# Optimization experiments

Hardware: AMD Instinct MI355X
Metric: run time of the kernel (lower is better)

## Reference

```python
import jax, jax.numpy as jnp
import numpy as np

B, NIN, NOUT, E = 4, 50000, 50000, 819200
CIN, COUT, H = 16, 16, 100


def _lin(key, fan_in, fan_out):
    k1, k2 = jax.random.split(key)
    s = 1.0 / np.sqrt(fan_in)
    w = jax.random.uniform(k1, (fan_in, fan_out), jnp.float32, -s, s)
    b = jax.random.uniform(k2, (fan_out,), jnp.float32, -s, s)
    return w, b


def setup_inputs() -> dict:
    key = jax.random.key(0)
    ks = jax.random.split(key, 12)
    inp = {}
    inp["x"] = jax.random.normal(ks[0], (B, NIN * CIN), jnp.float32)
    inp["inp_positions"] = jax.random.uniform(ks[1], (NIN, 3), jnp.float32)
    inp["out_positions"] = jax.random.uniform(ks[2], (NOUT, 3), jnp.float32)
    inp["edge_src"] = jax.random.randint(ks[3], (E,), 0, NIN)
    inp["edge_dst"] = jax.random.randint(ks[4], (E,), 0, NOUT)
    # edge-MLP: Linear(6,100) -> ReLU -> Linear(100,100) -> ReLU -> Linear(100,100) -> ReLU -> Linear(100, CIN*COUT)
    inp["w1"], inp["b1"] = _lin(ks[5], 6, H)
    inp["w2"], inp["b2"] = _lin(ks[6], H, H)
    inp["w3"], inp["b3"] = _lin(ks[7], H, H)
    inp["w4"], inp["b4"] = _lin(ks[8], H, CIN * COUT)
    inp["root"], _ = _lin(ks[9], CIN, COUT)  # NNConv root weight
    inp["bias"] = jax.random.uniform(ks[10], (COUT,), jnp.float32, -0.05, 0.05)
    return inp


def reference(x, inp_positions, out_positions, w1, b1, w2, b2, w3, b3, w4, b4, root, bias, edge_src, edge_dst):
    # x: (B, NIN*CIN) -> node features of input nodes; output nodes get zero features
    xb = x.reshape(B, NIN, CIN)
    # edge attributes: cat(out_pos[dst], in_pos[src]) -> (E, 6)
    e_attr = jnp.concatenate([out_positions[edge_dst], inp_positions[edge_src]], axis=1)
    # per-edge MLP producing edge-conditioned weight matrix (E, CIN, COUT)
    h = jax.nn.relu(e_attr @ w1 + b1)
    h = jax.nn.relu(h @ w2 + b2)
    h = jax.nn.relu(h @ w3 + b3)
    W = (h @ w4 + b4).reshape(E, CIN, COUT)
    # gather source features, apply edge-specific matmul -> messages (E, B, COUT)
    x_src = xb[:, edge_src]  # (B, E, CIN)
    msg = jnp.einsum('bei,eio->ebo', x_src, W)
    # mean-aggregate into destination (output) nodes
    agg = jax.ops.segment_sum(msg.reshape(E, B * COUT), edge_dst, num_segments=NOUT)
    deg = jax.ops.segment_sum(jnp.ones((E,), jnp.float32), edge_dst, num_segments=NOUT)
    agg = (agg / jnp.clip(deg, 1.0)[:, None]).reshape(NOUT, B, COUT)
    # root-weight term: destination node features are zeros -> contributes zero; bias remains
    out = jnp.transpose(agg, (1, 0, 2)) + bias  # (B, NOUT, COUT)
    return out
```

## Files before the change

### kernel.cpp

```cpp
#include <hip/hip_runtime.h>
#include <hip/hip_bf16.h>
#include <cstdint>

constexpr int B_    = 4;
constexpr int NIN_  = 50000;
constexpr int NOUT_ = 50000;
constexpr int E_    = 819200;
constexpr int CI    = 16;
constexpr int CO    = 16;
constexpr int Hh    = 100;

constexpr int NBLK   = 256;
constexpr int BITER  = E_ / 512;
constexpr size_t LDS_BYTES = 163840;

typedef __attribute__((ext_vector_type(8))) short bf16x8;
typedef __attribute__((ext_vector_type(4))) float f32x4;

union frag { bf16x8 v; unsigned u[4]; };

__device__ inline unsigned pk2(float a, float b) {
    unsigned r;
    asm("v_cvt_pk_bf16_f32 %0, %1, %2" : "=v"(r) : "v"(a), "v"(b));
    return r;
}

__device__ inline int chunkXor(int r) { return ((r & 7) << 3) ^ ((r & 8) << 1); }
__device__ inline int swz(int r, int k) { return r * 128 + (k ^ chunkXor(r)); }


__global__ __launch_bounds__(256)
void prep_kernel(const float* __restrict__ w1, const float* __restrict__ w2,
                 const float* __restrict__ w3, const float* __restrict__ w4,
                 const float* __restrict__ b1, const float* __restrict__ b2,
                 const float* __restrict__ b3, const float* __restrict__ b4,
                 unsigned short* __restrict__ wcat, unsigned short* __restrict__ W1T,
                 float* __restrict__ b1p, float* __restrict__ b2p,
                 float* __restrict__ b3p, float* __restrict__ b4p)
{
    const int i = blockIdx.x * 256 + threadIdx.x;
    auto bf = [](float f) {
        __hip_bfloat16 h = __float2bfloat16(f);
        return *reinterpret_cast<unsigned short*>(&h);
    };
    auto inv = [](int kpos) {
        return ((kpos >> 2) & 1) * 64 + ((kpos >> 5) & 3) * 16 +
               ((kpos >> 3) & 3) * 4 + (kpos & 3);
    };
    if (i < 32768) {
        int j = i & 16383; int r = j >> 7, kz = j & 127;
        int kpos = kz ^ chunkXor(r);
        int u = inv(kpos);
        const float* w = (i < 16384) ? w2 : w3;
        wcat[i] = (r < Hh && u < Hh) ? bf(w[u * Hh + r]) : (unsigned short)0;
    } else if (i < 65536) {
        int j = i - 32768; int r = j >> 7, kz = j & 127;
        int kpos = kz ^ chunkXor(r);
        int u = inv(kpos);
        wcat[i] = (u < Hh) ? bf(w4[u * 256 + r]) : (unsigned short)0;
    } else if (i < 69632) {
        int j = i - 65536; int wi = j >> 5, k = j & 31;
        W1T[j] = (k < 6 && wi < Hh) ? bf(w1[k * Hh + wi]) : (unsigned short)0;
    } else if (i < 69760) { int j = i - 69632; b1p[j] = (j < Hh) ? b1[j] : 0.f; }
    else if (i < 69888) { int j = i - 69760; b2p[j] = (j < Hh) ? b2[j] : 0.f; }
    else if (i < 70016) { int j = i - 69888; b3p[j] = (j < Hh) ? b3[j] : 0.f; }
    else if (i < 70272) { int j = i - 70016; b4p[j] = b4[j]; }
}

__global__ __launch_bounds__(256)
void packx_kernel(const float* __restrict__ x, uint4* __restrict__ xbf4)
{
    const int s = blockIdx.x * 256 + threadIdx.x;
    if (s >= NIN_) return;
    float4 r[4][4];
    #pragma unroll
    for (int b = 0; b < 4; ++b) {
        const float* xp = x + ((size_t)b * NIN_ + s) * CI;
        #pragma unroll
        for (int q = 0; q < 4; ++q)
            r[b][q] = *reinterpret_cast<const float4*>(xp + q * 4);
    }
    #pragma unroll
    for (int p = 0; p < 8; ++p) {
        const int q = p >> 1;
        const int h = (p & 1) * 2;
        uint4 v;
        v.x = pk2(((const float*)&r[0][q])[h],     ((const float*)&r[1][q])[h]);
        v.y = pk2(((const float*)&r[2][q])[h],     ((const float*)&r[3][q])[h]);
        v.z = pk2(((const float*)&r[0][q])[h + 1], ((const float*)&r[1][q])[h + 1]);
        v.w = pk2(((const float*)&r[2][q])[h + 1], ((const float*)&r[3][q])[h + 1]);
        xbf4[(size_t)s * 8 + p] = v;
    }
}

__device__ inline void hidden_layer4(const unsigned short* __restrict__ Wl,
                                     const float* __restrict__ bp,
                                     const frag (&in)[4][4], frag (&out)[4][4],
                                     int cl, int kg)
{
    #pragma unroll
    for (int nt = 0; nt < 8; ++nt) {
        bf16x8 wf[4];
        #pragma unroll
        for (int ks = 0; ks < 4; ++ks)
            wf[ks] = *reinterpret_cast<const bf16x8*>(
                Wl + swz(nt * 16 + cl, ks * 32 + kg * 8));
        f32x4 bias = *reinterpret_cast<const f32x4*>(bp + nt * 16 + kg * 4);
        #pragma unroll
        for (int et = 0; et < 4; ++et) {
            f32x4 acc = bias;
            #pragma unroll
            for (int ks = 0; ks < 4; ++ks)
                acc = __builtin_amdgcn_mfma_f32_16x16x32_bf16(wf[ks], in[et][ks].v, acc, 0, 0, 0);
            out[et][nt & 3].u[((nt >> 2) << 1) + 0] = pk2(fmaxf(acc[0], 0.f), fmaxf(acc[1], 0.f));
            out[et][nt & 3].u[((nt >> 2) << 1) + 1] = pk2(fmaxf(acc[2], 0.f), fmaxf(acc[3], 0.f));
        }
    }
}

__global__ __launch_bounds__(512)
__attribute__((amdgpu_waves_per_eu(2, 2)))
void edge_kernel(const uint4* __restrict__ xbf4, const float* __restrict__ ipos,
                 const float* __restrict__ opos, const int* __restrict__ esrc,
                 const int* __restrict__ edst,
                 const unsigned short* __restrict__ wcat,
                 const unsigned short* __restrict__ W1T,
                 const float* __restrict__ b1p, const float* __restrict__ b2p,
                 const float* __restrict__ b3p, const float* __restrict__ b4p,
                 float* __restrict__ agg, float* __restrict__ deg)
{
    extern __shared__ char lds[];
    unsigned short* Wlds = (unsigned short*)lds;

    const int tid  = threadIdx.x;
    const int wv   = __builtin_amdgcn_readfirstlane(tid >> 6);
    const int lane = tid & 63;
    const int cl   = lane & 15;
    const int kg   = lane >> 4;

    int srcv, dstv; unsigned au0, au1, au2;
    {
        const int eA = (blockIdx.x * 8 + wv) * 64 + lane;
        srcv = esrc[eA]; dstv = edst[eA];
        atomicAdd(&deg[dstv], 1.0f);
        float o0 = opos[dstv * 3 + 0], o1 = opos[dstv * 3 + 1], o2 = opos[dstv * 3 + 2];
        float i0 = ipos[srcv * 3 + 0], i1 = ipos[srcv * 3 + 1], i2 = ipos[srcv * 3 + 2];
        au0 = pk2(o0, o1); au1 = pk2(o2, i0); au2 = pk2(i1, i2);
    }

    {
        const float4* s4 = (const float4*)wcat;
        float4* d4 = (float4*)lds;
        for (int i = tid; i < 8192; i += 512) d4[i] = s4[i];
    }
    __syncthreads();

    uint2* xs = (uint2*)(lds + 131072 + wv * 4096);

    for (int bt = blockIdx.x; bt < BITER; bt += NBLK) {
        uint4 xq[8];
        {
            const uint4* xp = xbf4 + (size_t)srcv * 8;
            #pragma unroll
            for (int p = 0; p < 8; ++p) xq[p] = xp[p];
        }
        bf16x8 a1w[8];
        #pragma unroll
        for (int nt = 0; nt < 8; ++nt)
            a1w[nt] = *reinterpret_cast<const bf16x8*>(
                W1T + (nt * 16 + cl) * 32 + kg * 8);

        frag b1f[4];
        #pragma unroll
        for (int et = 0; et < 4; ++et) {
            const int sl = et * 16 + cl;
            unsigned s0 = __shfl(au0, sl), s1 = __shfl(au1, sl), s2 = __shfl(au2, sl);
            frag f;
            f.u[0] = (kg == 0) ? s0 : 0u;
            f.u[1] = (kg == 0) ? s1 : 0u;
            f.u[2] = (kg == 0) ? s2 : 0u;
            f.u[3] = 0u;
            b1f[et] = f;
        }

        frag B2[4][4];
        #pragma unroll
        for (int nt = 0; nt < 8; ++nt) {
            f32x4 bias = *reinterpret_cast<const f32x4*>(b1p + nt * 16 + kg * 4);
            #pragma unroll
            for (int et = 0; et < 4; ++et) {
                f32x4 acc = bias;
                acc = __builtin_amdgcn_mfma_f32_16x16x32_bf16(a1w[nt], b1f[et].v, acc, 0, 0, 0);
                B2[et][nt & 3].u[((nt >> 2) << 1) + 0] = pk2(fmaxf(acc[0], 0.f), fmaxf(acc[1], 0.f));
                B2[et][nt & 3].u[((nt >> 2) << 1) + 1] = pk2(fmaxf(acc[2], 0.f), fmaxf(acc[3], 0.f));
            }
        }

        int nsrc = srcv, ndst = dstv;
        unsigned na0 = au0, na1 = au1, na2 = au2;
        {
            const int nbt = bt + NBLK;
            if (nbt < BITER) {
                const int neA = (nbt * 8 + wv) * 64 + lane;
                nsrc = esrc[neA]; ndst = edst[neA];
                atomicAdd(&deg[ndst], 1.0f);
                float o0 = opos[ndst * 3 + 0], o1 = opos[ndst * 3 + 1], o2 = opos[ndst * 3 + 2];
                float i0 = ipos[nsrc * 3 + 0], i1 = ipos[nsrc * 3 + 1], i2 = ipos[nsrc * 3 + 2];
                na0 = pk2(o0, o1); na1 = pk2(o2, i0); na2 = pk2(i1, i2);
            }
        }

        frag B3[4][4];
        hidden_layer4(Wlds, b2p, B2, B3, cl, kg);
        frag B4[4][4];
        hidden_layer4(Wlds + 16384, b3p, B3, B4, cl, kg);

        float macc[4][16];
        #pragma unroll
        for (int et = 0; et < 4; ++et)
            #pragma unroll
            for (int q = 0; q < 16; ++q) macc[et][q] = 0.f;

        const unsigned short* W4l = Wlds + 32768;

        #pragma unroll
        for (int p = 0; p < 4; ++p) {
            xs[(2 * p + 0) * 64 + lane] = make_uint2(xq[p].x, xq[p].y);
            xs[(2 * p + 1) * 64 + lane] = make_uint2(xq[p].z, xq[p].w);
        }
        #pragma unroll
        for (int nt = 0; nt < 8; ++nt) {
            bf16x8 wf[4];
            #pragma unroll
            for (int ks = 0; ks < 4; ++ks)
                wf[ks] = *reinterpret_cast<const bf16x8*>(
                    W4l + swz(nt * 16 + cl, ks * 32 + kg * 8));
            const float bv = b4p[nt * 16 + cl];
            #pragma unroll
            for (int et = 0; et < 4; ++et) {
                const uint4 xa = *reinterpret_cast<const uint4*>(
                    &xs[nt * 64 + et * 16 + kg * 4]);
                const uint4 xb = *reinterpret_cast<const uint4*>(
                    &xs[nt * 64 + et * 16 + kg * 4 + 2]);
                f32x4 acc = {bv, bv, bv, bv};
                #pragma unroll
                for (int ks = 0; ks < 4; ++ks)
                    acc = __builtin_amdgcn_mfma_f32_16x16x32_bf16(B4[et][ks].v, wf[ks], acc, 0, 0, 0);
                const unsigned w01b[4] = {xa.x, xa.z, xb.x, xb.z};
                const unsigned w23b[4] = {xa.y, xa.w, xb.y, xb.w};
                #pragma unroll
                for (int j = 0; j < 4; ++j) {
                    const float x0 = __uint_as_float(w01b[j] << 16);
                    const float x1 = __uint_as_float(w01b[j] & 0xffff0000u);
                    const float x2 = __uint_as_float(w23b[j] << 16);
                    const float x3 = __uint_as_float(w23b[j] & 0xffff0000u);
                    macc[et][0 * 4 + j] = fmaf(x0, acc[j], macc[et][0 * 4 + j]);
                    macc[et][1 * 4 + j] = fmaf(x1, acc[j], macc[et][1 * 4 + j]);
                    macc[et][2 * 4 + j] = fmaf(x2, acc[j], macc[et][2 * 4 + j]);
                    macc[et][3 * 4 + j] = fmaf(x3, acc[j], macc[et][3 * 4 + j]);
                }
            }
        }

        #pragma unroll
        for (int p = 0; p < 4; ++p) {
            xs[(2 * p + 0) * 64 + lane] = make_uint2(xq[4 + p].x, xq[4 + p].y);
            xs[(2 * p + 1) * 64 + lane] = make_uint2(xq[4 + p].z, xq[4 + p].w);
        }
        #pragma unroll
        for (int nt8 = 0; nt8 < 8; ++nt8) {
            const int nt = 8 + nt8;
            bf16x8 wf[4];
            #pragma unroll
            for (int ks = 0; ks < 4; ++ks)
                wf[ks] = *reinterpret_cast<const bf16x8*>(
                    W4l + swz(nt * 16 + cl, ks * 32 + kg * 8));
            const float bv = b4p[nt * 16 + cl];
            #pragma unroll
            for (int et = 0; et < 4; ++et) {
                const uint4 xa = *reinterpret_cast<const uint4*>(
                    &xs[nt8 * 64 + et * 16 + kg * 4]);
                const uint4 xb = *reinterpret_cast<const uint4*>(
                    &xs[nt8 * 64 + et * 16 + kg * 4 + 2]);
                f32x4 acc = {bv, bv, bv, bv};
                #pragma unroll
                for (int ks = 0; ks < 4; ++ks)
                    acc = __builtin_amdgcn_mfma_f32_16x16x32_bf16(B4[et][ks].v, wf[ks], acc, 0, 0, 0);
                const unsigned w01b[4] = {xa.x, xa.z, xb.x, xb.z};
                const unsigned w23b[4] = {xa.y, xa.w, xb.y, xb.w};
                #pragma unroll
                for (int j = 0; j < 4; ++j) {
                    const float x0 = __uint_as_float(w01b[j] << 16);
                    const float x1 = __uint_as_float(w01b[j] & 0xffff0000u);
                    const float x2 = __uint_as_float(w23b[j] << 16);
                    const float x3 = __uint_as_float(w23b[j] & 0xffff0000u);
                    macc[et][0 * 4 + j] = fmaf(x0, acc[j], macc[et][0 * 4 + j]);
                    macc[et][1 * 4 + j] = fmaf(x1, acc[j], macc[et][1 * 4 + j]);
                    macc[et][2 * 4 + j] = fmaf(x2, acc[j], macc[et][2 * 4 + j]);
                    macc[et][3 * 4 + j] = fmaf(x3, acc[j], macc[et][3 * 4 + j]);
                }
            }
        }

        #pragma unroll
        for (int et = 0; et < 4; ++et)
            #pragma unroll
            for (int j = 0; j < 4; ++j) {
                const int d = __shfl(dstv, et * 16 + kg * 4 + j);
                #pragma unroll
                for (int b = 0; b < 4; ++b)
                    atomicAdd(agg + (size_t)b * (NOUT_ * CO) + (size_t)d * CO + cl,
                              macc[et][b * 4 + j]);
            }

        srcv = nsrc; dstv = ndst; au0 = na0; au1 = na1; au2 = na2;
    }
}

__global__ __launch_bounds__(256)
void finalize_kernel(const float* __restrict__ agg, const float* __restrict__ deg,
                     const float* __restrict__ bias, float* __restrict__ out)
{
    const int idx4 = blockIdx.x * 256 + threadIdx.x;
    const int n = (idx4 >> 2) % NOUT_;
    const float4 a = reinterpret_cast<const float4*>(agg)[idx4];
    const float dinv = 1.0f / fmaxf(deg[n], 1.0f);
    const float4 bv = reinterpret_cast<const float4*>(bias)[idx4 & 3];
    float4 o;
    o.x = a.x * dinv + bv.x;
    o.y = a.y * dinv + bv.y;
    o.z = a.z * dinv + bv.z;
    o.w = a.w * dinv + bv.w;
    reinterpret_cast<float4*>(out)[idx4] = o;
}

extern "C" void kernel_launch(void* const* d_in, const int* in_sizes, int n_in,
                              void* d_out, int out_size, void* d_ws, size_t ws_size,
                              hipStream_t stream)
{
    const float* x    = (const float*)d_in[0];
    const float* ipos = (const float*)d_in[1];
    const float* opos = (const float*)d_in[2];
    const int*   esrc = (const int*)d_in[3];
    const int*   edst = (const int*)d_in[4];
    const float* w1   = (const float*)d_in[5];
    const float* b1   = (const float*)d_in[6];
    const float* w2   = (const float*)d_in[7];
    const float* b2   = (const float*)d_in[8];
    const float* w3   = (const float*)d_in[9];
    const float* b3   = (const float*)d_in[10];
    const float* w4   = (const float*)d_in[11];
    const float* b4   = (const float*)d_in[12];
    const float* bias = (const float*)d_in[14];

    char* ob = (char*)d_out;
    unsigned short* wcat = (unsigned short*)ob;
    unsigned short* W1T  = (unsigned short*)(ob + 131072);
    float* b1p = (float*)(ob + 139264);
    float* b2p = (float*)(ob + 139776);
    float* b3p = (float*)(ob + 140288);
    float* b4p = (float*)(ob + 140800);
    uint4* xbf4 = (uint4*)(ob + 147456);

    float* agg = (float*)d_ws;
    float* deg = agg + (size_t)B_ * NOUT_ * CO;

    hipMemsetAsync(d_ws, 0,
                   ((size_t)B_ * NOUT_ * CO + NOUT_) * sizeof(float), stream);

    prep_kernel<<<275, 256, 0, stream>>>(w1, w2, w3, w4, b1, b2, b3, b4,
                                         wcat, W1T, b1p, b2p, b3p, b4p);
    packx_kernel<<<(NIN_ + 255) / 256, 256, 0, stream>>>(x, xbf4);

    hipFuncSetAttribute(reinterpret_cast<const void*>(edge_kernel),
                        hipFuncAttributeMaxDynamicSharedMemorySize,
                        (int)LDS_BYTES);
    edge_kernel<<<NBLK, 512, LDS_BYTES, stream>>>(
        xbf4, ipos, opos, esrc, edst, wcat, W1T, b1p, b2p, b3p, b4p, agg, deg);

    finalize_kernel<<<B_ * NOUT_ * CO / 4 / 256, 256, 0, stream>>>(
        agg, deg, bias, (float*)d_out);
}
```

Before: 363.0 us.

## Stream W4 from global memory to halve LDS and double occupancy

Only the W2/W3 weights are now staged in LDS, and the last-layer weight W4 is read straight from global memory (through the cache), which cuts the LDS footprint in half. That allows twice as many blocks (NBLK 512) and waves_per_eu 4. The per-wave x staging buffer shrinks to a 4-row ring that is refilled chunk by chunk. The trade-off is a lower register budget per wave, with possible spills, plus W4 fragment loads that now come from global/L1 instead of LDS.

```diff
diff --git a/kernel.cpp b/kernel.cpp
--- a/kernel.cpp
+++ b/kernel.cpp
@@ -10,9 +10,9 @@
 constexpr int CO    = 16;
 constexpr int Hh    = 100;
 
-constexpr int NBLK   = 256;
+constexpr int NBLK   = 512;
 constexpr int BITER  = E_ / 512;
-constexpr size_t LDS_BYTES = 163840;
+constexpr size_t LDS_BYTES = 81920;
 
 typedef __attribute__((ext_vector_type(8))) short bf16x8;
 typedef __attribute__((ext_vector_type(4))) float f32x4;
@@ -119,7 +119,7 @@
 }
 
 __global__ __launch_bounds__(512)
-__attribute__((amdgpu_waves_per_eu(2, 2)))
+__attribute__((amdgpu_waves_per_eu(4, 4)))
 void edge_kernel(const uint4* __restrict__ xbf4, const float* __restrict__ ipos,
                  const float* __restrict__ opos, const int* __restrict__ esrc,
                  const int* __restrict__ edst,
@@ -151,11 +151,12 @@
     {
         const float4* s4 = (const float4*)wcat;
         float4* d4 = (float4*)lds;
-        for (int i = tid; i < 8192; i += 512) d4[i] = s4[i];
+        for (int i = tid; i < 4096; i += 512) d4[i] = s4[i];
     }
     __syncthreads();
 
-    uint2* xs = (uint2*)(lds + 131072 + wv * 4096);
+    uint2* xs = (uint2*)(lds + 65536 + wv * 2048);
+    const unsigned short* W4g = wcat + 32768;
 
     for (int bt = blockIdx.x; bt < BITER; bt += NBLK) {
         uint4 xq[8];
@@ -221,83 +222,49 @@
             #pragma unroll
             for (int q = 0; q < 16; ++q) macc[et][q] = 0.f;
 
-        const unsigned short* W4l = Wlds + 32768;
-
-        #pragma unroll
-        for (int p = 0; p < 4; ++p) {
-            xs[(2 * p + 0) * 64 + lane] = make_uint2(xq[p].x, xq[p].y);
-            xs[(2 * p + 1) * 64 + lane] = make_uint2(xq[p].z, xq[p].w);
-        }
-        #pragma unroll
-        for (int nt = 0; nt < 8; ++nt) {
-            bf16x8 wf[4];
-            #pragma unroll
-            for (int ks = 0; ks < 4; ++ks)
-                wf[ks] = *reinterpret_cast<const bf16x8*>(
-                    W4l + swz(nt * 16 + cl, ks * 32 + kg * 8));
-            const float bv = b4p[nt * 16 + cl];
-            #pragma unroll
-            for (int et = 0; et < 4; ++et) {
-                const uint4 xa = *reinterpret_cast<const uint4*>(
-                    &xs[nt * 64 + et * 16 + kg * 4]);
-                const uint4 xb = *reinterpret_cast<const uint4*>(
-                    &xs[nt * 64 + et * 16 + kg * 4 + 2]);
-                f32x4 acc = {bv, bv, bv, bv};
+        xs[0 * 64 + lane] = make_uint2(xq[0].x, xq[0].y);
+        xs[1 * 64 + lane] = make_uint2(xq[0].z, xq[0].w);
+
+        #pragma unroll
+        for (int c = 0; c < 8; ++c) {
+            if (c < 7) {
+                const int r0 = 2 * ((c + 1) & 1);
+                xs[(r0 + 0) * 64 + lane] = make_uint2(xq[c + 1].x, xq[c + 1].y);
+                xs[(r0 + 1) * 64 + lane] = make_uint2(xq[c + 1].z, xq[c + 1].w);
+            }
+            #pragma unroll
+            for (int j2 = 0; j2 < 2; ++j2) {
+                const int nt = 2 * c + j2;
+                bf16x8 wf[4];
                 #pragma unroll
                 for (int ks = 0; ks < 4; ++ks)
-                    acc = __builtin_amdgcn_mfma_f32_16x16x32_bf16(B4[et][ks].v, wf[ks], acc, 0, 0, 0);
-                const unsigned w01b[4] = {xa.x, xa.z, xb.x, xb.z};
-                const unsigned w23b[4] = {xa.y, xa.w, xb.y, xb.w};
+                    wf[ks] = *reinterpret_cast<const bf16x8*>(
+                        W4g + swz(nt * 16 + cl, ks * 32 + kg * 8));
+                const float bv = b4p[nt * 16 + cl];
+                const int xrow = (nt & 3) * 64;
                 #pragma unroll
-                for (int j = 0; j < 4; ++j) {
-                    const float x0 = __uint_as_float(w01b[j] << 16);
-                    const float x1 = __uint_as_float(w01b[j] & 0xffff0000u);
-                    const float x2 = __uint_as_float(w23b[j] << 16);
-                    const float x3 = __uint_as_float(w23b[j] & 0xffff0000u);
-                    macc[et][0 * 4 + j] = fmaf(x0, acc[j], macc[et][0 * 4 + j]);
-                    macc[et][1 * 4 + j] = fmaf(x1, acc[j], macc[et][1 * 4 + j]);
-                    macc[et][2 * 4 + j] = fmaf(x2, acc[j], macc[et][2 * 4 + j]);
-                    macc[et][3 * 4 + j] = fmaf(x3, acc[j], macc[et][3 * 4 + j]);
-                }
-            }
-        }
-
-        #pragma unroll
-        for (int p = 0; p < 4; ++p) {
-            xs[(2 * p + 0) * 64 + lane] = make_uint2(xq[4 + p].x, xq[4 + p].y);
-            xs[(2 * p + 1) * 64 + lane] = make_uint2(xq[4 + p].z, xq[4 + p].w);
-        }
-        #pragma unroll
-        for (int nt8 = 0; nt8 < 8; ++nt8) {
-            const int nt = 8 + nt8;
-            bf16x8 wf[4];
-            #pragma unroll
-            for (int ks = 0; ks < 4; ++ks)
-                wf[ks] = *reinterpret_cast<const bf16x8*>(
-                    W4l + swz(nt * 16 + cl, ks * 32 + kg * 8));
-            const float bv = b4p[nt * 16 + cl];
-            #pragma unroll
-            for (int et = 0; et < 4; ++et) {
-                const uint4 xa = *reinterpret_cast<const uint4*>(
-                    &xs[nt8 * 64 + et * 16 + kg * 4]);
-                const uint4 xb = *reinterpret_cast<const uint4*>(
-                    &xs[nt8 * 64 + et * 16 + kg * 4 + 2]);
-                f32x4 acc = {bv, bv, bv, bv};
-                #pragma unroll
-                for (int ks = 0; ks < 4; ++ks)
-                    acc = __builtin_amdgcn_mfma_f32_16x16x32_bf16(B4[et][ks].v, wf[ks], acc, 0, 0, 0);
-                const unsigned w01b[4] = {xa.x, xa.z, xb.x, xb.z};
-                const unsigned w23b[4] = {xa.y, xa.w, xb.y, xb.w};
-                #pragma unroll
-                for (int j = 0; j < 4; ++j) {
-                    const float x0 = __uint_as_float(w01b[j] << 16);
-                    const float x1 = __uint_as_float(w01b[j] & 0xffff0000u);
-                    const float x2 = __uint_as_float(w23b[j] << 16);
-                    const float x3 = __uint_as_float(w23b[j] & 0xffff0000u);
-                    macc[et][0 * 4 + j] = fmaf(x0, acc[j], macc[et][0 * 4 + j]);
-                    macc[et][1 * 4 + j] = fmaf(x1, acc[j], macc[et][1 * 4 + j]);
-                    macc[et][2 * 4 + j] = fmaf(x2, acc[j], macc[et][2 * 4 + j]);
-                    macc[et][3 * 4 + j] = fmaf(x3, acc[j], macc[et][3 * 4 + j]);
+                for (int et = 0; et < 4; ++et) {
+                    const uint4 xa = *reinterpret_cast<const uint4*>(
+                        &xs[xrow + et * 16 + kg * 4]);
+                    const uint4 xb = *reinterpret_cast<const uint4*>(
+                        &xs[xrow + et * 16 + kg * 4 + 2]);
+                    f32x4 acc = {bv, bv, bv, bv};
+                    #pragma unroll
+                    for (int ks = 0; ks < 4; ++ks)
+                        acc = __builtin_amdgcn_mfma_f32_16x16x32_bf16(B4[et][ks].v, wf[ks], acc, 0, 0, 0);
+                    const unsigned w01b[4] = {xa.x, xa.z, xb.x, xb.z};
+                    const unsigned w23b[4] = {xa.y, xa.w, xb.y, xb.w};
+                    #pragma unroll
+                    for (int j = 0; j < 4; ++j) {
+                        const float x0 = __uint_as_float(w01b[j] << 16);
+                        const float x1 = __uint_as_float(w01b[j] & 0xffff0000u);
+                        const float x2 = __uint_as_float(w23b[j] << 16);
+                        const float x3 = __uint_as_float(w23b[j] & 0xffff0000u);
+                        macc[et][0 * 4 + j] = fmaf(x0, acc[j], macc[et][0 * 4 + j]);
+                        macc[et][1 * 4 + j] = fmaf(x1, acc[j], macc[et][1 * 4 + j]);
+                        macc[et][2 * 4 + j] = fmaf(x2, acc[j], macc[et][2 * 4 + j]);
+                        macc[et][3 * 4 + j] = fmaf(x3, acc[j], macc[et][3 * 4 + j]);
+                    }
                 }
             }
         }
```

Result: slower. 1.247 ms (+243.7%).
